# Kernel optimization log

Measured on AMD Instinct MI355X. Metric: run time of the kernel, lower is better.

## Reference

```python
import jax, jax.numpy as jnp
from jax import lax
import numpy as np

ALIGN = 6                 # AlignW: pad width up to a multiple of align_width=6
W_BITS = 5
A_BITS = 5
A_MASK = (1 << A_BITS) - 1  # direct_conv2d bit-packs activations: keep low A_bits
DN = ('NCHW', 'OIHW', 'NCHW')


def _align_w(a):
    pad = (-a.shape[-1]) % ALIGN
    if pad:
        a = jnp.pad(a, ((0, 0), (0, 0), (0, 0), (0, pad)))
    return a


def _conv_relu(a, w, b):
    # nn.Conv2d(kernel_size=3, padding=2) + ReLU
    y = lax.conv_general_dilated(a, w, (1, 1), [(2, 2), (2, 2)], dimension_numbers=DN)
    return jax.nn.relu(y + b[None, :, None, None])


def _dc_conv(a, w):
    # DC_layer: integer direct conv2d, W_bits-quantized weights, A_bits activations,
    # stride 1, no padding (valid).
    aq = jnp.bitwise_and(a, A_MASK)
    return lax.conv_general_dilated(aq, w, (1, 1), [(0, 0), (0, 0)], dimension_numbers=DN,
                                    preferred_element_type=jnp.int32)


def _maxpool2(a):
    if jnp.issubdtype(a.dtype, jnp.floating):
        init = np.float32(-np.inf)
    else:
        init = np.int32(np.iinfo(np.int32).min)
    return lax.reduce_window(a, init, lax.max, (1, 1, 2, 2), (1, 1, 2, 2), 'VALID')


def _forward(x, ws, bs, qs, fc_w, fc_b):
    a = x
    k = 0
    for n in (2, 2, 3):          # float VGG blocks: [64,64,M, 128,128,M, 256,256,256,M]
        for _ in range(n):
            a = _conv_relu(_align_w(a), ws[k], bs[k])
            k += 1
        a = _maxpool2(a)
    # dequant stub is identity; x.int() truncates toward zero (a >= 0 after ReLU)
    xi = lax.stop_gradient(a).astype(jnp.int32)
    k = 0
    for n in (3, 3):             # DC blocks: [512,512,512,M, 512,512,512,M]
        for _ in range(n):
            xi = _dc_conv(_align_w(xi), qs[k])
            k += 1
        xi = _maxpool2(xi)
    # classifier: AdaptiveAvgPool2d((1,1)) + Flatten + Linear(512, 1000)
    pooled = jnp.mean(xi.astype(jnp.float32), axis=(2, 3))
    return pooled @ fc_w.T + fc_b


def setup_inputs() -> dict:
    key = jax.random.key(0)
    ks = jax.random.split(key, 24)
    d = {}
    d['x'] = jax.random.uniform(ks[0], (16, 3, 224, 224), jnp.float32) * 8.0
    conv_cfg = [(3, 64), (64, 64), (64, 128), (128, 128), (128, 256), (256, 256), (256, 256)]
    for i, (ci, co) in enumerate(conv_cfg):
        d[f'w{i + 1}'] = jax.random.normal(ks[1 + i], (co, ci, 3, 3), jnp.float32) * 0.1
        d[f'b{i + 1}'] = jax.random.normal(ks[8 + i], (co,), jnp.float32) * 0.1
    dc_cfg = [(256, 512)] + [(512, 512)] * 5
    for i, (ci, co) in enumerate(dc_cfg):
        # torch.randint(0, 2**W_bits - 1, ...) -> values in [0, 2**W_bits - 2]
        d[f'q{i + 1}'] = jax.random.randint(ks[15 + i], (co, ci, 3, 3), 0, 2 ** W_BITS - 1, jnp.int32)
    d['fc_w'] = jax.random.normal(ks[21], (1000, 512), jnp.float32) * 0.02
    d['fc_b'] = jnp.zeros((1000,), jnp.float32)
    return d


def reference(x, w1, w2, w3, w4, w5, w6, w7,
              b1, b2, b3, b4, b5, b6, b7,
              q1, q2, q3, q4, q5, q6, fc_w, fc_b):
    ws = (w1, w2, w3, w4, w5, w6, w7)
    bs = (b1, b2, b3, b4, b5, b6, b7)
    qs = (q1, q2, q3, q4, q5, q6)
    return _forward(x, ws, bs, qs, fc_w, fc_b)
```

## Files before the change

### kernel.cpp

```cpp
#include <hip/hip_runtime.h>
#include <cstddef>


typedef float v2f __attribute__((ext_vector_type(2)));

static __device__ __forceinline__ int dot4(int a, int b, int c) {
#if __has_builtin(__builtin_amdgcn_sdot4)
    return __builtin_amdgcn_sdot4(a, b, c, false);
#else
    return c + (a & 255) * (b & 255)
             + ((a >> 8) & 255) * ((b >> 8) & 255)
             + ((a >> 16) & 255) * ((b >> 16) & 255)
             + ((a >> 24) & 255) * ((b >> 24) & 255);
#endif
}

static __device__ __forceinline__ void ld6f(const float* __restrict__ p, float v[6]) {
    const float4 a = *reinterpret_cast<const float4*>(p);
    const float2 b = *reinterpret_cast<const float2*>(p + 4);
    v[0] = a.x; v[1] = a.y; v[2] = a.z; v[3] = a.w; v[4] = b.x; v[5] = b.y;
}
static __device__ __forceinline__ void ld6i(const int* __restrict__ p, int v[6]) {
    const int4 a = *reinterpret_cast<const int4*>(p);
    const int2 b = *reinterpret_cast<const int2*>(p + 4);
    v[0] = a.x; v[1] = a.y; v[2] = a.z; v[3] = a.w; v[4] = b.x; v[5] = b.y;
}

static __device__ __forceinline__ void fmac8(const float v[3][6],
                                             const float* __restrict__ wr,
                                             v2f acc[8][2])
{
#pragma unroll
    for (int kh = 0; kh < 3; ++kh) {
        const v2f P0 = {v[kh][0], v[kh][1]};
        const v2f P1 = {v[kh][1], v[kh][2]};
        const v2f P2 = {v[kh][2], v[kh][3]};
        const v2f Q1 = {v[kh][3], v[kh][4]};
        const v2f Q2 = {v[kh][4], v[kh][5]};
#pragma unroll
        for (int c = 0; c < 8; ++c) {
            const float k0 = wr[c * 9 + kh * 3 + 0];
            const float k1 = wr[c * 9 + kh * 3 + 1];
            const float k2 = wr[c * 9 + kh * 3 + 2];
            const v2f k0p = {k0, k0}, k1p = {k1, k1}, k2p = {k2, k2};
            v2f a0 = acc[c][0];
            a0 = __builtin_elementwise_fma(P2, k2p, a0);
            a0 = __builtin_elementwise_fma(P1, k1p, a0);
            a0 = __builtin_elementwise_fma(P0, k0p, a0);
            acc[c][0] = a0;
            v2f a1 = acc[c][1];
            a1 = __builtin_elementwise_fma(Q2, k2p, a1);
            a1 = __builtin_elementwise_fma(Q1, k1p, a1);
            a1 = __builtin_elementwise_fma(P2, k0p, a1);
            acc[c][1] = a1;
        }
    }
}

static __device__ __forceinline__ void fmac4p(const float v[4][6],
                                              const float* __restrict__ wr,
                                              v2f acc[4][2][2])
{
#pragma unroll
    for (int r = 0; r < 2; ++r) {
#pragma unroll
        for (int kh = 0; kh < 3; ++kh) {
            const float* vv = v[r + kh];
            const v2f P0 = {vv[0], vv[1]};
            const v2f P1 = {vv[1], vv[2]};
            const v2f P2 = {vv[2], vv[3]};
            const v2f Q1 = {vv[3], vv[4]};
            const v2f Q2 = {vv[4], vv[5]};
#pragma unroll
            for (int c = 0; c < 4; ++c) {
                const float k0 = wr[c * 9 + kh * 3 + 0];
                const float k1 = wr[c * 9 + kh * 3 + 1];
                const float k2 = wr[c * 9 + kh * 3 + 2];
                const v2f k0p = {k0, k0}, k1p = {k1, k1}, k2p = {k2, k2};
                v2f a0 = acc[c][r][0];
                a0 = __builtin_elementwise_fma(P2, k2p, a0);
                a0 = __builtin_elementwise_fma(P1, k1p, a0);
                a0 = __builtin_elementwise_fma(P0, k0p, a0);
                acc[c][r][0] = a0;
                v2f a1 = acc[c][r][1];
                a1 = __builtin_elementwise_fma(Q2, k2p, a1);
                a1 = __builtin_elementwise_fma(Q1, k1p, a1);
                a1 = __builtin_elementwise_fma(P2, k0p, a1);
                acc[c][r][1] = a1;
            }
        }
    }
}

static __device__ __forceinline__ void dotc8(const int v[3][6],
                                             const int* __restrict__ wr,
                                             int acc[8][4])
{
#pragma unroll
    for (int kh = 0; kh < 3; ++kh) {
#pragma unroll
        for (int c = 0; c < 8; ++c) {
            const int k0 = wr[c * 9 + kh * 3 + 0];
            const int k1 = wr[c * 9 + kh * 3 + 1];
            const int k2 = wr[c * 9 + kh * 3 + 2];
#pragma unroll
            for (int t = 0; t < 4; ++t)
                acc[c][t] = dot4(v[kh][t], k0,
                            dot4(v[kh][t + 1], k1,
                            dot4(v[kh][t + 2], k2, acc[c][t])));
        }
    }
}

template<int CIN,int PH,int PW,int OH,int OW,int OPW,bool BORDER>
__global__ __launch_bounds__(256) void convf_k(
    const float* __restrict__ in, int instr,
    const float* __restrict__ wfp, const float* __restrict__ bias,
    float* __restrict__ out, int outstr, int total)
{
    constexpr int WB  = (OW + 3) / 4;
    constexpr int OPH = BORDER ? OH + 4 : OH;
    constexpr int OPL = OPH * OPW;
    const int s = blockIdx.z * 256 + threadIdx.x;
    if (s >= total) return;
    const int wb = s % WB;
    const int h  = (s / WB) % OH;
    const int n  = s / (WB * OH);
    const int w0 = wb * 4;
    const int cob = blockIdx.x;
    const int co0 = cob * 8;

    const float* ip = in + (size_t)n * instr + (size_t)h * PW + w0;
    const float* wl = wfp + (size_t)cob * CIN * 72;

    v2f acc[8][2];
#pragma unroll
    for (int c = 0; c < 8; ++c) { acc[c][0] = (v2f)0.f; acc[c][1] = (v2f)0.f; }

    float vb[3][6], vn[3][6];
#pragma unroll
    for (int kh = 0; kh < 3; ++kh) ld6f(ip + kh * PW, vb[kh]);

    if constexpr ((CIN & 1) == 0) {
        for (int ci = 0; ci < CIN; ci += 2) {
            ip += PH * PW;
#pragma unroll
            for (int kh = 0; kh < 3; ++kh) ld6f(ip + kh * PW, vn[kh]);
            fmac8(vb, wl + (size_t)ci * 72, acc);
            ip += PH * PW;
#pragma unroll
            for (int kh = 0; kh < 3; ++kh) ld6f(ip + kh * PW, vb[kh]);
            fmac8(vn, wl + (size_t)(ci + 1) * 72, acc);
        }
    } else {
        for (int ci = 0; ci < CIN; ++ci) {
            ip += PH * PW;
#pragma unroll
            for (int kh = 0; kh < 3; ++kh) ld6f(ip + kh * PW, vn[kh]);
            fmac8(vb, wl + (size_t)ci * 72, acc);
#pragma unroll
            for (int kh = 0; kh < 3; ++kh)
#pragma unroll
                for (int j = 0; j < 6; ++j) vb[kh][j] = vn[kh][j];
        }
    }

    float* ob = out + (size_t)n * outstr;
    const int ph  = BORDER ? h + 2 : h;
    const int pwo = BORDER ? 2 : 0;
#pragma unroll
    for (int c = 0; c < 8; ++c) {
        float* plane = ob + (size_t)(co0 + c) * OPL;
        float* row = plane + (size_t)ph * OPW;
        const float b = bias[co0 + c];
        float av[4] = {acc[c][0][0], acc[c][0][1], acc[c][1][0], acc[c][1][1]};
#pragma unroll
        for (int t = 0; t < 4; ++t)
            if (w0 + t < OW) { const float r = av[t] + b; row[pwo + w0 + t] = r > 0.f ? r : 0.f; }
        if (BORDER) {
            if (wb == 0) { row[0] = 0.f; row[1] = 0.f; }
            if (wb == WB - 1) { for (int pw = OW + 2; pw < OPW; ++pw) row[pw] = 0.f; }
            if (h == 0 || h == OH - 1) {
                float* r0 = plane + (h == 0 ? 0 : (size_t)(OH + 2) * OPW);
                for (int rr = 0; rr < 2; ++rr) {
                    float* br = r0 + (size_t)rr * OPW;
#pragma unroll
                    for (int t = 0; t < 4; ++t) if (w0 + t < OW) br[2 + w0 + t] = 0.f;
                    if (wb == 0) { br[0] = 0.f; br[1] = 0.f; }
                    if (wb == WB - 1) { for (int pw = OW + 2; pw < OPW; ++pw) br[pw] = 0.f; }
                }
            }
        }
    }
}

template<int CIN,int PH,int PW,int POH,int POW,int OPW,int OY,int OX,bool TOINT>
__global__ __launch_bounds__(256) void convfp_k(
    const float* __restrict__ in, int instr,
    const float* __restrict__ wfp, const float* __restrict__ bias,
    void* __restrict__ outv, int outstr, int total)
{
    constexpr int WBp = POW / 2;
    constexpr int OPH = POH + 2 * OY;
    constexpr int OPL = OPH * OPW;
    const int s = blockIdx.z * 256 + threadIdx.x;
    if (s >= total) return;
    const int pb = s % WBp;
    const int ph = (s / WBp) % POH;
    const int n  = s / (WBp * POH);
    const int cob = blockIdx.x;
    const int co0 = cob * 4;

    const float* ip = in + (size_t)n * instr + (size_t)(2 * ph) * PW + 4 * pb;
    const float* wl = wfp + (size_t)cob * CIN * 36;

    v2f acc[4][2][2];
#pragma unroll
    for (int c = 0; c < 4; ++c)
#pragma unroll
        for (int r = 0; r < 2; ++r) { acc[c][r][0] = (v2f)0.f; acc[c][r][1] = (v2f)0.f; }

    float vb[4][6], vn[4][6];
#pragma unroll
    for (int r = 0; r < 4; ++r) ld6f(ip + r * PW, vb[r]);

    for (int ci = 0; ci < CIN; ci += 2) {
        ip += PH * PW;
#pragma unroll
        for (int r = 0; r < 4; ++r) ld6f(ip + r * PW, vn[r]);
        fmac4p(vb, wl + (size_t)ci * 36, acc);
        ip += PH * PW;
#pragma unroll
        for (int r = 0; r < 4; ++r) ld6f(ip + r * PW, vb[r]);
        fmac4p(vn, wl + (size_t)(ci + 1) * 36, acc);
    }

#pragma unroll
    for (int c = 0; c < 4; ++c) {
        const float b = bias[co0 + c];
        float r00 = acc[c][0][0][0] + b; r00 = r00 > 0.f ? r00 : 0.f;
        float r01 = acc[c][0][0][1] + b; r01 = r01 > 0.f ? r01 : 0.f;
        float r02 = acc[c][0][1][0] + b; r02 = r02 > 0.f ? r02 : 0.f;
        float r03 = acc[c][0][1][1] + b; r03 = r03 > 0.f ? r03 : 0.f;
        float r10 = acc[c][1][0][0] + b; r10 = r10 > 0.f ? r10 : 0.f;
        float r11 = acc[c][1][0][1] + b; r11 = r11 > 0.f ? r11 : 0.f;
        float r12 = acc[c][1][1][0] + b; r12 = r12 > 0.f ? r12 : 0.f;
        float r13 = acc[c][1][1][1] + b; r13 = r13 > 0.f ? r13 : 0.f;
        float p0 = r00; p0 = p0 > r01 ? p0 : r01; p0 = p0 > r10 ? p0 : r10; p0 = p0 > r11 ? p0 : r11;
        float p1 = r02; p1 = p1 > r03 ? p1 : r03; p1 = p1 > r12 ? p1 : r12; p1 = p1 > r13 ? p1 : r13;

        if constexpr (TOINT) {
            int* plane = (int*)outv + (size_t)n * outstr + (size_t)(co0 + c) * OPL;
            int* row = plane + (size_t)(OY + ph) * OPW;
            row[OX + 2 * pb]     = (int)p0;
            row[OX + 2 * pb + 1] = (int)p1;
            if (pb == WBp - 1) { for (int pw = OX + POW; pw < OPW; ++pw) row[pw] = 0; }
        } else {
            float* plane = (float*)outv + (size_t)n * outstr + (size_t)(co0 + c) * OPL;
            float* row = plane + (size_t)(OY + ph) * OPW;
            row[OX + 2 * pb]     = p0;
            row[OX + 2 * pb + 1] = p1;
            if (OX > 0 && pb == 0) { row[0] = 0.f; row[1] = 0.f; }
            if (pb == WBp - 1) { for (int pw = OX + POW; pw < OPW; ++pw) row[pw] = 0.f; }
            if (OY > 0 && (ph == 0 || ph == POH - 1)) {
                float* r0 = plane + (ph == 0 ? 0 : (size_t)(OY + POH) * OPW);
                for (int rr = 0; rr < OY; ++rr) {
                    float* br = r0 + (size_t)rr * OPW;
                    br[OX + 2 * pb] = 0.f; br[OX + 2 * pb + 1] = 0.f;
                    if (pb == 0) { br[0] = 0.f; br[1] = 0.f; }
                    if (pb == WBp - 1) { for (int pw = OX + POW; pw < OPW; ++pw) br[pw] = 0.f; }
                }
            }
        }
    }
}

template<int CIN4,int PH,int PW,int OH,int OW,int OPW,bool PACKOUT>
__global__ __launch_bounds__(256) void convq_k(
    const int* __restrict__ in, int instr, const int* __restrict__ wqp,
    int* __restrict__ out, int outstr, int total)
{
    constexpr int WB  = (OW + 3) / 4;
    constexpr int OPL = OH * OPW;
    const int s = blockIdx.z * 256 + threadIdx.x;
    if (s >= total) return;
    const int wb = s % WB;
    const int h  = (s / WB) % OH;
    const int n  = s / (WB * OH);
    const int w0 = wb * 4;
    const int cob = blockIdx.x;
    const int co0 = cob * 8;

    const int* ip = in + (size_t)n * instr + (size_t)h * PW + w0;
    const int* wl = wqp + (size_t)cob * CIN4 * 72;

    int acc[8][4];
#pragma unroll
    for (int c = 0; c < 8; ++c)
#pragma unroll
        for (int t = 0; t < 4; ++t) acc[c][t] = 0;

    int vb[3][6], vn[3][6];
#pragma unroll
    for (int kh = 0; kh < 3; ++kh) ld6i(ip + kh * PW, vb[kh]);

    for (int ci = 0; ci < CIN4; ci += 2) {
        ip += PH * PW;
#pragma unroll
        for (int kh = 0; kh < 3; ++kh) ld6i(ip + kh * PW, vn[kh]);
        dotc8(vb, wl + (size_t)ci * 72, acc);
        ip += PH * PW;
#pragma unroll
        for (int kh = 0; kh < 3; ++kh) ld6i(ip + kh * PW, vb[kh]);
        dotc8(vn, wl + (size_t)(ci + 1) * 72, acc);
    }

    if (PACKOUT) {
        int* base = out + (size_t)n * outstr + (size_t)(cob * 2) * OPL + (size_t)h * OPW + w0;
#pragma unroll
        for (int t = 0; t < 4; ++t) {
            if (w0 + t < OW) {
                const int lo = (acc[0][t] & 31) | ((acc[1][t] & 31) << 8)
                             | ((acc[2][t] & 31) << 16) | ((acc[3][t] & 31) << 24);
                const int hi = (acc[4][t] & 31) | ((acc[5][t] & 31) << 8)
                             | ((acc[6][t] & 31) << 16) | ((acc[7][t] & 31) << 24);
                base[t] = lo;
                base[OPL + t] = hi;
            }
        }
        if (wb == WB - 1) {
            for (int pw = OW; pw < OPW; ++pw) { base[pw - w0] = 0; base[OPL + pw - w0] = 0; }
        }
    } else {
        int* ob = out + (size_t)n * outstr;
#pragma unroll
        for (int c = 0; c < 8; ++c) {
            int* row = ob + (size_t)(co0 + c) * OPL + (size_t)h * OPW;
#pragma unroll
            for (int t = 0; t < 4; ++t)
                if (w0 + t < OW) row[w0 + t] = acc[c][t];
            if (wb == WB - 1) { for (int pw = OW; pw < OPW; ++pw) row[pw] = 0; }
        }
    }
}

__global__ void pack_wf_k(const float* __restrict__ w, float* __restrict__ out,
                          int CIN, int TC, int total)
{
    const int i = blockIdx.x * 256 + threadIdx.x;
    if (i >= total) return;
    const int r = i % 9;
    const int c = (i / 9) % TC;
    const int t = i / (9 * TC);
    const int ci = t % CIN;
    const int cob = t / CIN;
    out[i] = w[(((size_t)cob * TC + c) * CIN + ci) * 9 + r];
}

__global__ void pack_wq_k(const int* __restrict__ q, int* __restrict__ out,
                          int CIN4, int total)
{
    const int i = blockIdx.x * 256 + threadIdx.x;
    if (i >= total) return;
    const int r = i % 9;
    const int c = (i / 9) % 8;
    const int t = i / 72;
    const int ci4 = t % CIN4;
    const int cob = t / CIN4;
    const int co = cob * 8 + c;
    const int* p = q + ((size_t)co * CIN4 * 4 + ci4 * 4) * 9 + r;
    out[i] = (p[0] & 255) | ((p[9] & 255) << 8) | ((p[18] & 255) << 16) | ((p[27] & 255) << 24);
}

template<int CIN,int PH,int PW>
__global__ void pack_a_k(const int* __restrict__ in, int instr,
                         int* __restrict__ out, int outstr, int total)
{
    const int i = blockIdx.x * 256 + threadIdx.x;
    if (i >= total) return;
    constexpr int CIN4 = CIN / 4;
    constexpr int PL = PH * PW;
    int t = i;
    const int pw = t % PW; t /= PW;
    const int ph = t % PH; t /= PH;
    const int c4 = t % CIN4; const int n = t / CIN4;
    const int* p = in + (size_t)n * instr + ((size_t)(c4 * 4) * PH + ph) * PW + pw;
    out[(size_t)n * outstr + ((size_t)c4 * PH + ph) * PW + pw] =
        (p[0] & 31) | ((p[PL] & 31) << 8) | ((p[2 * PL] & 31) << 16) | ((p[3 * PL] & 31) << 24);
}

template<int C,int HI,int WI,int HO,int WO,int OPH,int OPW>
__global__ void pool_i_k(const int* __restrict__ in, int instr,
                         int* __restrict__ out, int outstr, int total)
{
    const int i = blockIdx.x * 256 + threadIdx.x;
    if (i >= total) return;
    constexpr int OPL = OPH * OPW;
    int t = i;
    const int px = t % OPW; t /= OPW;
    const int py = t % OPH; t /= OPH;
    const int c  = t % C;   const int n = t / C;
    int v = 0;
    if (py < HO && px < WO) {
        const int* p = in + (size_t)n * instr + ((size_t)c * HI + 2 * py) * WI + 2 * px;
        int m = p[0];
        m = m > p[1] ? m : p[1];
        m = m > p[WI] ? m : p[WI];
        m = m > p[WI + 1] ? m : p[WI + 1];
        v = m;
    }
    out[(size_t)n * outstr + (size_t)c * OPL + (size_t)py * OPW + px] = v;
}

__global__ void copyin_k(const float* __restrict__ x, float* __restrict__ dst,
                         int outstr, int total)
{
    const int i = blockIdx.x * 256 + threadIdx.x;
    if (i >= total) return;
    int t = i;
    const int pw = t % 232; t /= 232;
    const int ph = t % 228; t /= 228;
    const int c  = t % 3;   const int n = t / 3;
    float v = 0.f;
    const int y = ph - 2, xx = pw - 2;
    if ((unsigned)y < 224u && (unsigned)xx < 224u)
        v = x[(size_t)n * 150528 + ((size_t)c * 224 + y) * 224 + xx];
    dst[(size_t)n * outstr + ((size_t)c * 228 + ph) * 232 + pw] = v;
}

__global__ void pool_mean_k(const int* __restrict__ in, int instr,
                            float* __restrict__ out, int outstr, int total)
{
    const int i = blockIdx.x * 256 + threadIdx.x;
    if (i >= total) return;
    const int n = i / 512, c = i % 512;
    const int* p = in + (size_t)n * instr + (size_t)c * 33;
    int s = 0;
#pragma unroll
    for (int j = 0; j < 33; ++j) s += p[j];
    out[(size_t)n * outstr + c] = (float)s / 33.0f;
}

__global__ void fc_k(const float* __restrict__ pooled, const float* __restrict__ w,
                     const float* __restrict__ b, float* __restrict__ out,
                     int nb, int n0)
{
    const int i = blockIdx.x * 256 + threadIdx.x;
    if (i >= nb * 1000) return;
    const int co = i % 1000;
    const int n  = i / 1000;
    const float* pv = pooled + (size_t)n * 512;
    const float* wr = w + (size_t)co * 512;
    float s = b[co];
    for (int c = 0; c < 512; ++c) s = fmaf(pv[c], wr[c], s);
    out[(size_t)(n0 + n) * 1000 + co] = s;
}

extern "C" void kernel_launch(void* const* d_in, const int* in_sizes, int n_in,
                              void* d_out, int out_size, void* d_ws, size_t ws_size,
                              hipStream_t stream)
{
    (void)n_in; (void)out_size;
    const float* x = (const float*)d_in[0];
    const float* W[7]; const float* Bv[7]; const int* Q[6];
    const bool inter = (in_sizes[2] == 64);
    for (int i = 0; i < 7; ++i) {
        if (inter) { W[i] = (const float*)d_in[1 + 2 * i]; Bv[i] = (const float*)d_in[2 + 2 * i]; }
        else       { W[i] = (const float*)d_in[1 + i];     Bv[i] = (const float*)d_in[8 + i];     }
    }
    for (int i = 0; i < 6; ++i) Q[i] = (const int*)d_in[15 + i];
    const float* fcw = (const float*)d_in[21];
    const float* fcb = (const float*)d_in[22];
    float* outp = (float*)d_out;

    static const int FCO[7]  = {64, 64, 128, 128, 256, 256, 256};
    static const int FCIN[7] = {3, 64, 64, 128, 128, 256, 256};
    static const int FTC[7]  = {8, 4, 8, 4, 8, 8, 4};
    static const int QCIN4[6] = {64, 128, 128, 128, 128, 128};
    size_t wfoff[7], wft = 0;
    for (int i = 0; i < 7; ++i) { wfoff[i] = wft; wft += (size_t)FCO[i] * FCIN[i] * 9; }
    size_t wqoff[6], wqt = 0;
    for (int i = 0; i < 6; ++i) { wqoff[i] = wqt; wqt += (size_t)512 * QCIN4[i] * 9 * 4; }
    const size_t WTOT = wft + wqt;

    float* wfb = (float*)d_ws;
    int*   wqb = (int*)((float*)d_ws + wft);
    for (int i = 0; i < 7; ++i) {
        const int total = FCO[i] * FCIN[i] * 9;
        pack_wf_k<<<(total + 255) / 256, 256, 0, stream>>>(W[i], wfb + wfoff[i], FCIN[i], FTC[i], total);
    }
    for (int i = 0; i < 6; ++i) {
        const int total = 512 * QCIN4[i] * 9;
        pack_wq_k<<<(total + 255) / 256, 256, 0, stream>>>(Q[i], wqb + wqoff[i], QCIN4[i], total);
    }

    const long long SZ_X0 = 158688,  SZ_F1 = 3532800, SZ_P1 = 936448;
    const long long SZ_F4 = 2027520, SZ_P2 = 580608,  SZ_F7 = 1264640;
    const long long SZ_F8 = 1440768, SZ_I0 = 360448,  SZ_PK1 = 90112;
    const long long SZ_D1 = 168960,  SZ_D2 = 157696,  SZ_D3 = 532480;
    const long long SZ_P4 = 159744,  SZ_PK4 = 39936,  SZ_D4 = 33792;
    const long long SZ_D5 = 27648,   SZ_D6 = 86016,   SZ_P5 = 16896;

    float* AR = (float*)d_ws + WTOT;
    long long AE2 = ((long long)(ws_size / 4) - (long long)WTOT - 20480) & ~3LL;

    int nbB = 16;
    for (;; nbB >>= 1) {
        if (nbB == 1) break;
        const long long f = nbB;
        const long long low = (nbB == 16) ? 0 : SZ_P1 * 16;
        const bool ok = (SZ_P1 * 16 + SZ_F4 * f <= AE2)
                     && (low + SZ_P2 * f <= AE2 - SZ_F4 * f)
                     && (low + SZ_F8 * f <= AE2 - SZ_F7 * f)
                     && (low + (SZ_PK1 + SZ_D1 + SZ_D2 + SZ_D3) * f <= AE2);
        if (ok) break;
    }
    int cA = 16;
    while (cA > 1 && SZ_P1 * 16 + (SZ_X0 + SZ_F1) * cA > AE2) cA >>= 1;

    const long long lowb = (nbB == 16) ? 0 : SZ_P1 * 16;
    float* tP1 = AR;
    float* tX0 = AR + SZ_P1 * 16;
    float* tF1 = tX0 + SZ_X0 * cA;
    float* tF4 = AR + (AE2 - SZ_F4 * nbB);
    float* tP2 = AR + lowb;
    float* tF7 = AR + (AE2 - SZ_F7 * nbB);
    float* tF8 = AR + lowb;
    int*   tI0 = (int*)(AR + (AE2 - SZ_I0 * nbB));
    int*   tPK1 = (int*)(AR + lowb);
    int*   tD1 = tPK1 + SZ_PK1 * nbB;
    int*   tD2 = tD1 + SZ_D1 * nbB;
    int*   tD3 = tD2 + SZ_D2 * nbB;
    int*   tP4 = (int*)(AR + lowb);
    int*   tPK4 = tP4 + SZ_P4 * nbB;
    int*   tD4 = tPK4 + SZ_PK4 * nbB;
    int*   tD5 = tD4 + SZ_D4 * nbB;
    int*   tD6 = tD5 + SZ_D5 * nbB;
    int*   tP5 = (int*)(AR + lowb);
    float* tPP = (float*)(tP5 + SZ_P5 * nbB);

    for (int a0 = 0; a0 < 16; a0 += cA) {
        const int nb = cA;
        {
            const int total = nb * 3 * 228 * 232;
            copyin_k<<<(total + 255) / 256, 256, 0, stream>>>(
                x + (size_t)a0 * 150528, tX0, (int)SZ_X0, total);
        }
        {
            const int total = nb * 226 * 58;
            dim3 g(8, 1, (total + 255) / 256);
            convf_k<3, 228, 232, 226, 230, 240, true><<<g, 256, 0, stream>>>(
                tX0, (int)SZ_X0, wfb + wfoff[0], Bv[0], tF1, (int)SZ_F1, total);
        }
        {
            const int total = nb * 114 * 59;
            dim3 g(16, 1, (total + 255) / 256);
            convfp_k<64, 230, 240, 114, 118, 124, 2, 2, false><<<g, 256, 0, stream>>>(
                tF1, (int)SZ_F1, wfb + wfoff[1], Bv[1],
                tP1 + (size_t)a0 * SZ_P1, (int)SZ_P1, total);
        }
    }

    for (int b0 = 0; b0 < 16; b0 += nbB) {
        const int nb = nbB;
        {
            const int total = nb * 116 * 31;
            dim3 g(16, 1, (total + 255) / 256);
            convf_k<64, 118, 124, 116, 122, 132, true><<<g, 256, 0, stream>>>(
                tP1 + (size_t)b0 * SZ_P1, (int)SZ_P1, wfb + wfoff[2], Bv[2],
                tF4, (int)SZ_F4, total);
        }
        {
            const int total = nb * 59 * 32;
            dim3 g(32, 1, (total + 255) / 256);
            convfp_k<128, 120, 132, 59, 64, 72, 2, 2, false><<<g, 256, 0, stream>>>(
                tF4, (int)SZ_F4, wfb + wfoff[3], Bv[3], tP2, (int)SZ_P2, total);
        }
        {
            const int total = nb * 61 * 17;
            dim3 g(32, 1, (total + 255) / 256);
            convf_k<128, 63, 72, 61, 68, 76, true><<<g, 256, 0, stream>>>(
                tP2, (int)SZ_P2, wfb + wfoff[4], Bv[4], tF7, (int)SZ_F7, total);
        }
        {
            const int total = nb * 63 * 19;
            dim3 g(32, 1, (total + 255) / 256);
            convf_k<256, 65, 76, 63, 74, 84, true><<<g, 256, 0, stream>>>(
                tF7, (int)SZ_F7, wfb + wfoff[5], Bv[5], tF8, (int)SZ_F8, total);
        }
        {
            const int total = nb * 32 * 20;
            dim3 g(64, 1, (total + 255) / 256);
            convfp_k<256, 67, 84, 32, 40, 44, 0, 0, true><<<g, 256, 0, stream>>>(
                tF8, (int)SZ_F8, wfb + wfoff[6], Bv[6], (void*)tI0, (int)SZ_I0, total);
        }
        {
            const int total = nb * 64 * 32 * 44;
            pack_a_k<256, 32, 44><<<(total + 255) / 256, 256, 0, stream>>>(
                tI0, (int)SZ_I0, tPK1, (int)SZ_PK1, total);
        }
        {
            const int total = nb * 30 * 10;
            dim3 g(64, 1, (total + 255) / 256);
            convq_k<64, 32, 44, 30, 40, 44, true><<<g, 256, 0, stream>>>(
                tPK1, (int)SZ_PK1, wqb + wqoff[0], tD1, (int)SZ_D1, total);
        }
        {
            const int total = nb * 28 * 10;
            dim3 g(64, 1, (total + 255) / 256);
            convq_k<128, 30, 44, 28, 40, 44, true><<<g, 256, 0, stream>>>(
                tD1, (int)SZ_D1, wqb + wqoff[1], tD2, (int)SZ_D2, total);
        }
        {
            const int total = nb * 26 * 10;
            dim3 g(64, 1, (total + 255) / 256);
            convq_k<128, 28, 44, 26, 40, 40, false><<<g, 256, 0, stream>>>(
                tD2, (int)SZ_D2, wqb + wqoff[2], tD3, (int)SZ_D3, total);
        }
        {
            const int total = nb * 512 * 13 * 24;
            pool_i_k<512, 26, 40, 13, 20, 13, 24><<<(total + 255) / 256, 256, 0, stream>>>(
                tD3, (int)SZ_D3, tP4, (int)SZ_P4, total);
        }
        {
            const int total = nb * 128 * 13 * 24;
            pack_a_k<512, 13, 24><<<(total + 255) / 256, 256, 0, stream>>>(
                tP4, (int)SZ_P4, tPK4, (int)SZ_PK4, total);
        }
        {
            const int total = nb * 11 * 6;
            dim3 g(64, 1, (total + 255) / 256);
            convq_k<128, 13, 24, 11, 22, 24, true><<<g, 256, 0, stream>>>(
                tPK4, (int)SZ_PK4, wqb + wqoff[3], tD4, (int)SZ_D4, total);
        }
        {
            const int total = nb * 9 * 6;
            dim3 g(64, 1, (total + 255) / 256);
            convq_k<128, 11, 24, 9, 22, 24, true><<<g, 256, 0, stream>>>(
                tD4, (int)SZ_D4, wqb + wqoff[4], tD5, (int)SZ_D5, total);
        }
        {
            const int total = nb * 7 * 6;
            dim3 g(64, 1, (total + 255) / 256);
            convq_k<128, 9, 24, 7, 22, 24, false><<<g, 256, 0, stream>>>(
                tD5, (int)SZ_D5, wqb + wqoff[5], tD6, (int)SZ_D6, total);
        }
        {
            const int total = nb * 512 * 33;
            pool_i_k<512, 7, 24, 3, 11, 3, 11><<<(total + 255) / 256, 256, 0, stream>>>(
                tD6, (int)SZ_D6, tP5, (int)SZ_P5, total);
        }
        {
            const int total = nb * 512;
            pool_mean_k<<<(total + 255) / 256, 256, 0, stream>>>(
                tP5, (int)SZ_P5, tPP, 512, total);
        }
        {
            const int total = nb * 1000;
            fc_k<<<(total + 255) / 256, 256, 0, stream>>>(tPP, fcw, fcb, outp, nb, b0);
        }
    }
}
```

Before: 5.998 ms.

## Fuse activation packing into conv/pool kernels and restructure row loads

The last float conv+pool kernel now writes bit-packed 5-bit activations directly, and a new poolpack kernel fuses the int maxpool with packing, removing two kernels and their intermediate buffers. Workspace layout is rearranged to match. Row loads now fetch an extra unaligned float4 so the shifted pairs come straight from memory instead of being built from register shuffles, and the explicit double-buffered channel loop becomes a plain loop with unroll 2. The FC kernel switches to float4 loads. The risk is that the compiler no longer overlaps the next channel's loads with the current FMAs, and the extra unaligned loads add memory traffic.

```diff
diff --git a/kernel.cpp b/kernel.cpp
--- a/kernel.cpp
+++ b/kernel.cpp
@@ -15,28 +15,31 @@
 #endif
 }
 
-static __device__ __forceinline__ void ld6f(const float* __restrict__ p, float v[6]) {
-    const float4 a = *reinterpret_cast<const float4*>(p);
-    const float2 b = *reinterpret_cast<const float2*>(p + 4);
-    v[0] = a.x; v[1] = a.y; v[2] = a.z; v[3] = a.w; v[4] = b.x; v[5] = b.y;
-}
+struct Rw { v2f a0, a1, a2, b0, b1; };
+
+static __device__ __forceinline__ Rw ldr(const float* __restrict__ p) {
+    Rw r;
+    const float4 x = *reinterpret_cast<const float4*>(p);
+    const float2 y = *reinterpret_cast<const float2*>(p + 4);
+    const float4 z = *reinterpret_cast<const float4*>(p + 1);
+    r.a0 = v2f{x.x, x.y}; r.a1 = v2f{x.z, x.w}; r.a2 = v2f{y.x, y.y};
+    r.b0 = v2f{z.x, z.y}; r.b1 = v2f{z.z, z.w};
+    return r;
+}
+
 static __device__ __forceinline__ void ld6i(const int* __restrict__ p, int v[6]) {
     const int4 a = *reinterpret_cast<const int4*>(p);
     const int2 b = *reinterpret_cast<const int2*>(p + 4);
     v[0] = a.x; v[1] = a.y; v[2] = a.z; v[3] = a.w; v[4] = b.x; v[5] = b.y;
 }
 
-static __device__ __forceinline__ void fmac8(const float v[3][6],
+static __device__ __forceinline__ void fmac8(const Rw v[3],
                                              const float* __restrict__ wr,
                                              v2f acc[8][2])
 {
 #pragma unroll
     for (int kh = 0; kh < 3; ++kh) {
-        const v2f P0 = {v[kh][0], v[kh][1]};
-        const v2f P1 = {v[kh][1], v[kh][2]};
-        const v2f P2 = {v[kh][2], v[kh][3]};
-        const v2f Q1 = {v[kh][3], v[kh][4]};
-        const v2f Q2 = {v[kh][4], v[kh][5]};
+        const Rw r = v[kh];
 #pragma unroll
         for (int c = 0; c < 8; ++c) {
             const float k0 = wr[c * 9 + kh * 3 + 0];
@@ -44,20 +47,20 @@
             const float k2 = wr[c * 9 + kh * 3 + 2];
             const v2f k0p = {k0, k0}, k1p = {k1, k1}, k2p = {k2, k2};
             v2f a0 = acc[c][0];
-            a0 = __builtin_elementwise_fma(P2, k2p, a0);
-            a0 = __builtin_elementwise_fma(P1, k1p, a0);
-            a0 = __builtin_elementwise_fma(P0, k0p, a0);
+            a0 = __builtin_elementwise_fma(r.a1, k2p, a0);
+            a0 = __builtin_elementwise_fma(r.b0, k1p, a0);
+            a0 = __builtin_elementwise_fma(r.a0, k0p, a0);
             acc[c][0] = a0;
             v2f a1 = acc[c][1];
-            a1 = __builtin_elementwise_fma(Q2, k2p, a1);
-            a1 = __builtin_elementwise_fma(Q1, k1p, a1);
-            a1 = __builtin_elementwise_fma(P2, k0p, a1);
+            a1 = __builtin_elementwise_fma(r.a2, k2p, a1);
+            a1 = __builtin_elementwise_fma(r.b1, k1p, a1);
+            a1 = __builtin_elementwise_fma(r.a1, k0p, a1);
             acc[c][1] = a1;
         }
     }
 }
 
-static __device__ __forceinline__ void fmac4p(const float v[4][6],
+static __device__ __forceinline__ void fmac4p(const Rw v[4],
                                               const float* __restrict__ wr,
                                               v2f acc[4][2][2])
 {
@@ -65,12 +68,7 @@
     for (int r = 0; r < 2; ++r) {
 #pragma unroll
         for (int kh = 0; kh < 3; ++kh) {
-            const float* vv = v[r + kh];
-            const v2f P0 = {vv[0], vv[1]};
-            const v2f P1 = {vv[1], vv[2]};
-            const v2f P2 = {vv[2], vv[3]};
-            const v2f Q1 = {vv[3], vv[4]};
-            const v2f Q2 = {vv[4], vv[5]};
+            const Rw rv = v[r + kh];
 #pragma unroll
             for (int c = 0; c < 4; ++c) {
                 const float k0 = wr[c * 9 + kh * 3 + 0];
@@ -78,14 +76,14 @@
                 const float k2 = wr[c * 9 + kh * 3 + 2];
                 const v2f k0p = {k0, k0}, k1p = {k1, k1}, k2p = {k2, k2};
                 v2f a0 = acc[c][r][0];
-                a0 = __builtin_elementwise_fma(P2, k2p, a0);
-                a0 = __builtin_elementwise_fma(P1, k1p, a0);
-                a0 = __builtin_elementwise_fma(P0, k0p, a0);
+                a0 = __builtin_elementwise_fma(rv.a1, k2p, a0);
+                a0 = __builtin_elementwise_fma(rv.b0, k1p, a0);
+                a0 = __builtin_elementwise_fma(rv.a0, k0p, a0);
                 acc[c][r][0] = a0;
                 v2f a1 = acc[c][r][1];
-                a1 = __builtin_elementwise_fma(Q2, k2p, a1);
-                a1 = __builtin_elementwise_fma(Q1, k1p, a1);
-                a1 = __builtin_elementwise_fma(P2, k0p, a1);
+                a1 = __builtin_elementwise_fma(rv.a2, k2p, a1);
+                a1 = __builtin_elementwise_fma(rv.b1, k1p, a1);
+                a1 = __builtin_elementwise_fma(rv.a1, k0p, a1);
                 acc[c][r][1] = a1;
             }
         }
@@ -137,32 +135,13 @@
 #pragma unroll
     for (int c = 0; c < 8; ++c) { acc[c][0] = (v2f)0.f; acc[c][1] = (v2f)0.f; }
 
-    float vb[3][6], vn[3][6];
-#pragma unroll
-    for (int kh = 0; kh < 3; ++kh) ld6f(ip + kh * PW, vb[kh]);
-
-    if constexpr ((CIN & 1) == 0) {
-        for (int ci = 0; ci < CIN; ci += 2) {
-            ip += PH * PW;
-#pragma unroll
-            for (int kh = 0; kh < 3; ++kh) ld6f(ip + kh * PW, vn[kh]);
-            fmac8(vb, wl + (size_t)ci * 72, acc);
-            ip += PH * PW;
-#pragma unroll
-            for (int kh = 0; kh < 3; ++kh) ld6f(ip + kh * PW, vb[kh]);
-            fmac8(vn, wl + (size_t)(ci + 1) * 72, acc);
-        }
-    } else {
-        for (int ci = 0; ci < CIN; ++ci) {
-            ip += PH * PW;
-#pragma unroll
-            for (int kh = 0; kh < 3; ++kh) ld6f(ip + kh * PW, vn[kh]);
-            fmac8(vb, wl + (size_t)ci * 72, acc);
-#pragma unroll
-            for (int kh = 0; kh < 3; ++kh)
-#pragma unroll
-                for (int j = 0; j < 6; ++j) vb[kh][j] = vn[kh][j];
-        }
+#pragma unroll 2
+    for (int ci = 0; ci < CIN; ++ci) {
+        Rw v[3];
+#pragma unroll
+        for (int kh = 0; kh < 3; ++kh) v[kh] = ldr(ip + kh * PW);
+        fmac8(v, wl + (size_t)ci * 72, acc);
+        ip += PH * PW;
     }
 
     float* ob = out + (size_t)n * outstr;
@@ -173,7 +152,7 @@
         float* plane = ob + (size_t)(co0 + c) * OPL;
         float* row = plane + (size_t)ph * OPW;
         const float b = bias[co0 + c];
-        float av[4] = {acc[c][0][0], acc[c][0][1], acc[c][1][0], acc[c][1][1]};
+        const float av[4] = {acc[c][0][0], acc[c][0][1], acc[c][1][0], acc[c][1][1]};
 #pragma unroll
         for (int t = 0; t < 4; ++t)
             if (w0 + t < OW) { const float r = av[t] + b; row[pwo + w0 + t] = r > 0.f ? r : 0.f; }
@@ -194,7 +173,7 @@
     }
 }
 
-template<int CIN,int PH,int PW,int POH,int POW,int OPW,int OY,int OX,bool TOINT>
+template<int CIN,int PH,int PW,int POH,int POW,int OPW,int OY,int OX,int MODE>
 __global__ __launch_bounds__(256) void convfp_k(
     const float* __restrict__ in, int instr,
     const float* __restrict__ wfp, const float* __restrict__ bias,
@@ -220,21 +199,16 @@
 #pragma unroll
         for (int r = 0; r < 2; ++r) { acc[c][r][0] = (v2f)0.f; acc[c][r][1] = (v2f)0.f; }
 
-    float vb[4][6], vn[4][6];
-#pragma unroll
-    for (int r = 0; r < 4; ++r) ld6f(ip + r * PW, vb[r]);
-
-    for (int ci = 0; ci < CIN; ci += 2) {
+#pragma unroll 2
+    for (int ci = 0; ci < CIN; ++ci) {
+        Rw v[4];
+#pragma unroll
+        for (int r = 0; r < 4; ++r) v[r] = ldr(ip + r * PW);
+        fmac4p(v, wl + (size_t)ci * 36, acc);
         ip += PH * PW;
-#pragma unroll
-        for (int r = 0; r < 4; ++r) ld6f(ip + r * PW, vn[r]);
-        fmac4p(vb, wl + (size_t)ci * 36, acc);
-        ip += PH * PW;
-#pragma unroll
-        for (int r = 0; r < 4; ++r) ld6f(ip + r * PW, vb[r]);
-        fmac4p(vn, wl + (size_t)(ci + 1) * 36, acc);
-    }
-
+    }
+
+    float p[4][2];
 #pragma unroll
     for (int c = 0; c < 4; ++c) {
         const float b = bias[co0 + c];
@@ -248,18 +222,28 @@
         float r13 = acc[c][1][1][1] + b; r13 = r13 > 0.f ? r13 : 0.f;
         float p0 = r00; p0 = p0 > r01 ? p0 : r01; p0 = p0 > r10 ? p0 : r10; p0 = p0 > r11 ? p0 : r11;
         float p1 = r02; p1 = p1 > r03 ? p1 : r03; p1 = p1 > r12 ? p1 : r12; p1 = p1 > r13 ? p1 : r13;
-
-        if constexpr (TOINT) {
-            int* plane = (int*)outv + (size_t)n * outstr + (size_t)(co0 + c) * OPL;
-            int* row = plane + (size_t)(OY + ph) * OPW;
-            row[OX + 2 * pb]     = (int)p0;
-            row[OX + 2 * pb + 1] = (int)p1;
-            if (pb == WBp - 1) { for (int pw = OX + POW; pw < OPW; ++pw) row[pw] = 0; }
-        } else {
+        p[c][0] = p0; p[c][1] = p1;
+    }
+
+    if constexpr (MODE == 1) {
+        int* base = (int*)outv + (size_t)n * outstr + (size_t)cob * OPL
+                  + (size_t)(OY + ph) * OPW + OX + 2 * pb;
+        base[0] = (((int)p[0][0]) & 31) | ((((int)p[1][0]) & 31) << 8)
+                | ((((int)p[2][0]) & 31) << 16) | ((((int)p[3][0]) & 31) << 24);
+        base[1] = (((int)p[0][1]) & 31) | ((((int)p[1][1]) & 31) << 8)
+                | ((((int)p[2][1]) & 31) << 16) | ((((int)p[3][1]) & 31) << 24);
+        if (pb == WBp - 1) {
+            int* row = (int*)outv + (size_t)n * outstr + (size_t)cob * OPL
+                     + (size_t)(OY + ph) * OPW;
+            for (int pw = OX + POW; pw < OPW; ++pw) row[pw] = 0;
+        }
+    } else {
+#pragma unroll
+        for (int c = 0; c < 4; ++c) {
             float* plane = (float*)outv + (size_t)n * outstr + (size_t)(co0 + c) * OPL;
             float* row = plane + (size_t)(OY + ph) * OPW;
-            row[OX + 2 * pb]     = p0;
-            row[OX + 2 * pb + 1] = p1;
+            row[OX + 2 * pb]     = p[c][0];
+            row[OX + 2 * pb + 1] = p[c][1];
             if (OX > 0 && pb == 0) { row[0] = 0.f; row[1] = 0.f; }
             if (pb == WBp - 1) { for (int pw = OX + POW; pw < OPW; ++pw) row[pw] = 0.f; }
             if (OY > 0 && (ph == 0 || ph == POH - 1)) {
@@ -372,21 +356,30 @@
     out[i] = (p[0] & 255) | ((p[9] & 255) << 8) | ((p[18] & 255) << 16) | ((p[27] & 255) << 24);
 }
 
-template<int CIN,int PH,int PW>
-__global__ void pack_a_k(const int* __restrict__ in, int instr,
-                         int* __restrict__ out, int outstr, int total)
+template<int C4,int HI,int WI,int HO,int WO,int OPH,int OPW>
+__global__ void poolpack_k(const int* __restrict__ in, int instr,
+                           int* __restrict__ out, int outstr, int total)
 {
     const int i = blockIdx.x * 256 + threadIdx.x;
     if (i >= total) return;
-    constexpr int CIN4 = CIN / 4;
-    constexpr int PL = PH * PW;
     int t = i;
-    const int pw = t % PW; t /= PW;
-    const int ph = t % PH; t /= PH;
-    const int c4 = t % CIN4; const int n = t / CIN4;
-    const int* p = in + (size_t)n * instr + ((size_t)(c4 * 4) * PH + ph) * PW + pw;
-    out[(size_t)n * outstr + ((size_t)c4 * PH + ph) * PW + pw] =
-        (p[0] & 31) | ((p[PL] & 31) << 8) | ((p[2 * PL] & 31) << 16) | ((p[3 * PL] & 31) << 24);
+    const int px = t % OPW; t /= OPW;
+    const int py = t % OPH; t /= OPH;
+    const int c4 = t % C4;  const int n = t / C4;
+    int word = 0;
+    if (py < HO && px < WO) {
+#pragma unroll
+        for (int j = 0; j < 4; ++j) {
+            const int* p = in + (size_t)n * instr
+                         + ((size_t)(c4 * 4 + j) * HI + 2 * py) * WI + 2 * px;
+            int m = p[0];
+            m = m > p[1] ? m : p[1];
+            m = m > p[WI] ? m : p[WI];
+            m = m > p[WI + 1] ? m : p[WI + 1];
+            word |= (m & 31) << (8 * j);
+        }
+    }
+    out[(size_t)n * outstr + ((size_t)c4 * OPH + py) * OPW + px] = word;
 }
 
 template<int C,int HI,int WI,int HO,int WO,int OPH,int OPW>
@@ -449,10 +442,14 @@
     if (i >= nb * 1000) return;
     const int co = i % 1000;
     const int n  = i / 1000;
-    const float* pv = pooled + (size_t)n * 512;
-    const float* wr = w + (size_t)co * 512;
+    const float4* pv = (const float4*)(pooled + (size_t)n * 512);
+    const float4* wr = (const float4*)(w + (size_t)co * 512);
     float s = b[co];
-    for (int c = 0; c < 512; ++c) s = fmaf(pv[c], wr[c], s);
+    for (int c = 0; c < 128; ++c) {
+        const float4 a = pv[c], q = wr[c];
+        s = fmaf(a.x, q.x, s); s = fmaf(a.y, q.y, s);
+        s = fmaf(a.z, q.z, s); s = fmaf(a.w, q.w, s);
+    }
     out[(size_t)(n0 + n) * 1000 + co] = s;
 }
 
@@ -496,10 +493,11 @@
 
     const long long SZ_X0 = 158688,  SZ_F1 = 3532800, SZ_P1 = 936448;
     const long long SZ_F4 = 2027520, SZ_P2 = 580608,  SZ_F7 = 1264640;
-    const long long SZ_F8 = 1440768, SZ_I0 = 360448,  SZ_PK1 = 90112;
+    const long long SZ_F8 = 1440768, SZ_PK1 = 90112;
     const long long SZ_D1 = 168960,  SZ_D2 = 157696,  SZ_D3 = 532480;
-    const long long SZ_P4 = 159744,  SZ_PK4 = 39936,  SZ_D4 = 33792;
-    const long long SZ_D5 = 27648,   SZ_D6 = 86016,   SZ_P5 = 16896;
+    const long long SZ_PK4 = 39936,  SZ_D4 = 33792,   SZ_D5 = 27648;
+    const long long SZ_D6 = 86016,   SZ_P5 = 16896;
+    const long long DCH = SZ_D1 + SZ_D2 + SZ_D3 + SZ_PK4 + SZ_D4 + SZ_D5 + SZ_D6 + SZ_P5 + 512;
 
     float* AR = (float*)d_ws + WTOT;
     long long AE2 = ((long long)(ws_size / 4) - (long long)WTOT - 20480) & ~3LL;
@@ -512,7 +510,8 @@
         const bool ok = (SZ_P1 * 16 + SZ_F4 * f <= AE2)
                      && (low + SZ_P2 * f <= AE2 - SZ_F4 * f)
                      && (low + SZ_F8 * f <= AE2 - SZ_F7 * f)
-                     && (low + (SZ_PK1 + SZ_D1 + SZ_D2 + SZ_D3) * f <= AE2);
+                     && (low + SZ_F8 * f <= AE2 - SZ_PK1 * f)
+                     && (low + DCH * f <= AE2 - SZ_PK1 * f);
         if (ok) break;
     }
     int cA = 16;
@@ -526,17 +525,15 @@
     float* tP2 = AR + lowb;
     float* tF7 = AR + (AE2 - SZ_F7 * nbB);
     float* tF8 = AR + lowb;
-    int*   tI0 = (int*)(AR + (AE2 - SZ_I0 * nbB));
-    int*   tPK1 = (int*)(AR + lowb);
-    int*   tD1 = tPK1 + SZ_PK1 * nbB;
+    int*   tPK1 = (int*)(AR + (AE2 - SZ_PK1 * nbB));
+    int*   tD1 = (int*)(AR + lowb);
     int*   tD2 = tD1 + SZ_D1 * nbB;
     int*   tD3 = tD2 + SZ_D2 * nbB;
-    int*   tP4 = (int*)(AR + lowb);
-    int*   tPK4 = tP4 + SZ_P4 * nbB;
+    int*   tPK4 = tD3 + SZ_D3 * nbB;
     int*   tD4 = tPK4 + SZ_PK4 * nbB;
     int*   tD5 = tD4 + SZ_D4 * nbB;
     int*   tD6 = tD5 + SZ_D5 * nbB;
-    int*   tP5 = (int*)(AR + lowb);
+    int*   tP5 = tD6 + SZ_D6 * nbB;
     float* tPP = (float*)(tP5 + SZ_P5 * nbB);
 
     for (int a0 = 0; a0 < 16; a0 += cA) {
@@ -555,7 +552,7 @@
         {
             const int total = nb * 114 * 59;
             dim3 g(16, 1, (total + 255) / 256);
-            convfp_k<64, 230, 240, 114, 118, 124, 2, 2, false><<<g, 256, 0, stream>>>(
+            convfp_k<64, 230, 240, 114, 118, 124, 2, 2, 0><<<g, 256, 0, stream>>>(
                 tF1, (int)SZ_F1, wfb + wfoff[1], Bv[1],
                 tP1 + (size_t)a0 * SZ_P1, (int)SZ_P1, total);
         }
@@ -573,7 +570,7 @@
         {
             const int total = nb * 59 * 32;
             dim3 g(32, 1, (total + 255) / 256);
-            convfp_k<128, 120, 132, 59, 64, 72, 2, 2, false><<<g, 256, 0, stream>>>(
+            convfp_k<128, 120, 132, 59, 64, 72, 2, 2, 0><<<g, 256, 0, stream>>>(
                 tF4, (int)SZ_F4, wfb + wfoff[3], Bv[3], tP2, (int)SZ_P2, total);
         }
         {
@@ -591,13 +588,8 @@
         {
             const int total = nb * 32 * 20;
             dim3 g(64, 1, (total + 255) / 256);
-            convfp_k<256, 67, 84, 32, 40, 44, 0, 0, true><<<g, 256, 0, stream>>>(
-                tF8, (int)SZ_F8, wfb + wfoff[6], Bv[6], (void*)tI0, (int)SZ_I0, total);
-        }
-        {
-            const int total = nb * 64 * 32 * 44;
-            pack_a_k<256, 32, 44><<<(total + 255) / 256, 256, 0, stream>>>(
-                tI0, (int)SZ_I0, tPK1, (int)SZ_PK1, total);
+            convfp_k<256, 67, 84, 32, 40, 44, 0, 0, 1><<<g, 256, 0, stream>>>(
+                tF8, (int)SZ_F8, wfb + wfoff[6], Bv[6], (void*)tPK1, (int)SZ_PK1, total);
         }
         {
             const int total = nb * 30 * 10;
@@ -618,14 +610,9 @@
                 tD2, (int)SZ_D2, wqb + wqoff[2], tD3, (int)SZ_D3, total);
         }
         {
-            const int total = nb * 512 * 13 * 24;
-            pool_i_k<512, 26, 40, 13, 20, 13, 24><<<(total + 255) / 256, 256, 0, stream>>>(
-                tD3, (int)SZ_D3, tP4, (int)SZ_P4, total);
-        }
-        {
             const int total = nb * 128 * 13 * 24;
-            pack_a_k<512, 13, 24><<<(total + 255) / 256, 256, 0, stream>>>(
-                tP4, (int)SZ_P4, tPK4, (int)SZ_PK4, total);
+            poolpack_k<128, 26, 40, 13, 20, 13, 24><<<(total + 255) / 256, 256, 0, stream>>>(
+                tD3, (int)SZ_D3, tPK4, (int)SZ_PK4, total);
         }
         {
             const int total = nb * 11 * 6;
```

Result: faster. 5.786 ms (-3.5%).
